# Kernel optimization log

Measured on AMD Instinct MI355X. Metric: run time of the kernel, lower is better.

The kernel has to match this reference:

```python
import jax, jax.numpy as jnp
import numpy as np

D_MODEL = 768
D_STATE = 16
K_CONV = 4
BATCH = 2
SEQ = 2048


def setup_inputs() -> dict:
    key = jax.random.key(0)
    ks = jax.random.split(key, 16)
    dm, ds, K = D_MODEL, D_STATE, K_CONV
    s = 0.02
    inp = {
        "x": jax.random.normal(ks[0], (BATCH, SEQ, dm), dtype=jnp.float32),
        # linear weights stored (in, out); y = x @ W + b (equivalent to torch Linear)
        "Wi": jax.random.normal(ks[1], (dm, 2 * dm), dtype=jnp.float32) * s,
        "bi": jnp.zeros((2 * dm,), jnp.float32),
        "Wconv": jax.random.normal(ks[2], (dm, K), dtype=jnp.float32) * s,
        "bconv": jnp.zeros((dm,), jnp.float32),
        "Wdt": jax.random.normal(ks[3], (dm, dm), dtype=jnp.float32) * s,
        "bdt": jnp.zeros((dm,), jnp.float32),
        "WB": jax.random.normal(ks[4], (dm, dm * ds), dtype=jnp.float32) * s,
        "bB": jnp.zeros((dm * ds,), jnp.float32),
        "WC": jax.random.normal(ks[5], (dm, dm * ds), dtype=jnp.float32) * s,
        "bC": jnp.zeros((dm * ds,), jnp.float32),
        "A_log": jnp.zeros((dm, ds), jnp.float32),  # matches nn.Parameter(torch.zeros)
        "D": jnp.ones((dm,), jnp.float32),          # matches nn.Parameter(torch.ones)
        "Wo": jax.random.normal(ks[6], (dm, dm), dtype=jnp.float32) * s,
        "bo": jnp.zeros((dm,), jnp.float32),
    }
    return inp


def _forward(x, Wi, bi, Wconv, bconv, Wdt, bdt, WB, bB, WC, bC, A_log, D, Wo, bo):
    B, L, dm = x.shape
    ds = A_log.shape[1]
    K = Wconv.shape[1]

    uv = x @ Wi + bi                        # (B, L, 2*dm)
    u, v = uv[..., :dm], uv[..., dm:]

    # causal depthwise conv1d: torch pads K-1 both sides, keeps first L outputs
    u_pad = jnp.pad(u, ((0, 0), (K - 1, 0), (0, 0)))
    u_conv = bconv + sum(u_pad[:, k:k + L, :] * Wconv[:, k] for k in range(K))

    dt = jax.nn.softplus(u_conv @ Wdt + bdt)            # (B, L, dm)
    Bt = (u_conv @ WB + bB).reshape(B, L, dm, ds)       # (B, L, dm, ds)
    Ct = (u_conv @ WC + bC).reshape(B, L, dm, ds)
    A = -jnp.exp(A_log)                                  # (dm, ds)

    def step(s, inputs):
        dt_t, u_t, B_tt, C_tt = inputs                   # (B,dm), (B,dm), (B,dm,ds), (B,dm,ds)
        dt_e = dt_t[..., None]
        s = s * jnp.exp(dt_e * A) + dt_e * B_tt * u_t[..., None]
        y = jnp.sum(C_tt * s, axis=-1) + D * u_t         # (B, dm)
        return s, y

    s0 = jnp.zeros((B, dm, ds), x.dtype)
    xs = (dt.transpose(1, 0, 2), u_conv.transpose(1, 0, 2),
          Bt.transpose(1, 0, 2, 3), Ct.transpose(1, 0, 2, 3))
    _, ys = jax.lax.scan(step, s0, xs)                   # ys: (L, B, dm)
    y = ys.transpose(1, 0, 2)

    y = y * jax.nn.sigmoid(v)
    return y @ Wo + bo


def reference(x, Wi, bi, Wconv, bconv, Wdt, bdt, WB, bB, WC, bC, A_log, D, Wo, bo):
    return _forward(x, Wi, bi, Wconv, bconv, Wdt, bdt, WB, bB, WC, bC, A_log, D, Wo, bo)
```

## Files before the change

### kernel.cpp

```cpp
#include <hip/hip_runtime.h>

#define DM 768
#define DS 16
#define SEQ 2048
#define BATCH 2
#define MROWS (BATCH*SEQ)
#define N_UV (2*DM)
#define N_BC (DM*DS)
#define NGRP (BATCH*DM/4)
#define SUBMAX 32

typedef _Float16 half8 __attribute__((ext_vector_type(8)));
typedef float floatx4 __attribute__((ext_vector_type(4)));

static __device__ __forceinline__ unsigned short f2h(float f) {
  _Float16 h = (_Float16)f;
  return __builtin_bit_cast(unsigned short, h);
}
static __device__ __forceinline__ float h2f(unsigned short u) {
  return (float)__builtin_bit_cast(_Float16, u);
}
static __device__ __forceinline__ float softplus_f(float x) {
  return (x > 20.f) ? x : log1pf(__expf(x));
}
static __device__ __forceinline__ void async_cp16(const unsigned short* g,
                                                  unsigned short* l) {
  __builtin_amdgcn_global_load_lds(
      (const __attribute__((address_space(1))) void*)g,
      (__attribute__((address_space(3))) void*)l, 16, 0, 0);
}
static __device__ __forceinline__ float row_reduce16(float v) {
  int x;
  x = __builtin_amdgcn_update_dpp(0, __builtin_bit_cast(int, v), 0x128, 0xf, 0xf, true);
  v += __builtin_bit_cast(float, x);
  x = __builtin_amdgcn_update_dpp(0, __builtin_bit_cast(int, v), 0x124, 0xf, 0xf, true);
  v += __builtin_bit_cast(float, x);
  x = __builtin_amdgcn_update_dpp(0, __builtin_bit_cast(int, v), 0x122, 0xf, 0xf, true);
  v += __builtin_bit_cast(float, x);
  x = __builtin_amdgcn_update_dpp(0, __builtin_bit_cast(int, v), 0x121, 0xf, 0xf, true);
  v += __builtin_bit_cast(float, x);
  return v;
}

__global__ void convert_f2h(const float* __restrict__ in,
                            unsigned short* __restrict__ out, int n) {
  int i = (blockIdx.x * blockDim.x + threadIdx.x) * 4;
  if (i >= n) return;
  float4 f = *(const float4*)(in + i);
  ushort4 h;
  h.x = f2h(f.x); h.y = f2h(f.y); h.z = f2h(f.z); h.w = f2h(f.w);
  *(ushort4*)(out + i) = h;
}

__global__ void transpose_f2h(const float* __restrict__ W,
                              unsigned short* __restrict__ WT, int K, int N) {
  __shared__ float tile[32][33];
  int n0 = blockIdx.x * 32, k0 = blockIdx.y * 32;
  int tx = threadIdx.x, ty = threadIdx.y;
#pragma unroll
  for (int i = 0; i < 32; i += 8)
    tile[ty + i][tx] = W[(size_t)(k0 + ty + i) * N + (n0 + tx)];
  __syncthreads();
#pragma unroll
  for (int i = 0; i < 32; i += 8)
    WT[(size_t)(n0 + ty + i) * K + (k0 + tx)] = f2h(tile[tx][ty + i]);
}

template<int ACT, int OUTH, int TRANS>
__global__ __launch_bounds__(256)
void gemm_f16(const unsigned short* __restrict__ A,
              const unsigned short* __restrict__ BT0,
              const unsigned short* __restrict__ BT1,
              const float* __restrict__ bias0,
              const float* __restrict__ bias1,
              void* __restrict__ Cout0,
              void* __restrict__ Cout1,
              int M, int N, int K, int TCa, int bstride, int row0, int ldT) {
  const unsigned short* BT = blockIdx.z ? BT1 : BT0;
  const float* bias = blockIdx.z ? bias1 : bias0;
  void* Cout = blockIdx.z ? Cout1 : Cout0;
  __shared__ __align__(16) unsigned short smem[2 * 128 * 32];
  unsigned short* As = smem;
  unsigned short* Bs = smem + 128 * 32;
  const int m0 = blockIdx.y * 128, n0 = blockIdx.x * 128;
  const int tid = threadIdx.x;
  const int lane = tid & 63, wave = tid >> 6;
  const int wm = (wave >> 1) * 64, wn = (wave & 1) * 64;
  const int l16 = lane & 15, quad = lane >> 4;
  const int sr = tid >> 2;
  const int sc = (((tid & 3) ^ ((tid >> 3) & 3))) * 8;
  const int pch = (quad ^ ((l16 >> 1) & 3)) * 8;

  floatx4 acc[4][4] = {};

  const int mA0 = m0 + sr, mA1 = m0 + sr + 64;
  const int gA0 = (mA0 / TCa) * bstride + row0 + (mA0 % TCa);
  const int gA1 = (mA1 / TCa) * bstride + row0 + (mA1 % TCa);
  const unsigned short* Arow0 = A + (size_t)gA0 * K + sc;
  const unsigned short* Arow1 = A + (size_t)gA1 * K + sc;
  const unsigned short* Brow0 = BT + (size_t)(n0 + sr) * K + sc;
  const unsigned short* Brow1 = BT + (size_t)(n0 + sr + 64) * K + sc;
  unsigned short* ldsA0 = As + (wave * 16) * 32;
  unsigned short* ldsA1 = As + (64 + wave * 16) * 32;
  unsigned short* ldsB0 = Bs + (wave * 16) * 32;
  unsigned short* ldsB1 = Bs + (64 + wave * 16) * 32;

  for (int k0 = 0; k0 < K; k0 += 32) {
    async_cp16(Arow0 + k0, ldsA0);
    async_cp16(Arow1 + k0, ldsA1);
    async_cp16(Brow0 + k0, ldsB0);
    async_cp16(Brow1 + k0, ldsB1);
    __syncthreads();
    half8 af[4], bf[4];
#pragma unroll
    for (int i = 0; i < 4; i++) {
      af[i] = __builtin_bit_cast(half8, *(const uint4*)&As[(wm + i * 16 + l16) * 32 + pch]);
      bf[i] = __builtin_bit_cast(half8, *(const uint4*)&Bs[(wn + i * 16 + l16) * 32 + pch]);
    }
#pragma unroll
    for (int mi = 0; mi < 4; mi++)
#pragma unroll
      for (int ni = 0; ni < 4; ni++)
        acc[mi][ni] = __builtin_amdgcn_mfma_f32_16x16x32_f16(af[mi], bf[ni], acc[mi][ni], 0, 0, 0);
    __syncthreads();
  }

  if (TRANS) {
#pragma unroll
    for (int ph = 0; ph < 2; ph++) {
      __syncthreads();
#pragma unroll
      for (int nn = 0; nn < 2; nn++) {
        int ni = ph * 2 + nn;
        int colb = wn + ni * 16 + l16;
        int cc = (wn >> 1) + nn * 16 + l16;
        float bv = bias[n0 + colb];
#pragma unroll
        for (int mi = 0; mi < 4; mi++) {
          int slot = (wm >> 2) + mi * 4 + quad;
          int pair = slot >> 1, bitb = slot & 1;
          int phys = ((pair ^ (cc & 15)) << 1) | bitb;
          union { _Float16 h[4]; unsigned long long u; } pk;
#pragma unroll
          for (int r = 0; r < 4; r++) {
            float v = acc[mi][ni][r] + bv;
            if (ACT == 1) v = softplus_f(v);
            pk.h[r] = (_Float16)v;
          }
          *(unsigned long long*)&smem[cc * 128 + phys * 4] = pk.u;
        }
      }
      __syncthreads();
#pragma unroll
      for (int pass = 0; pass < 4; pass++) {
        int cc = (tid >> 4) + pass * 16;
        int p16 = tid & 15;
        uint4 v = *(const uint4*)&smem[cc * 128 + (p16 ^ (cc & 15)) * 8];
        int colb = ((cc & 32) ? 64 : 0) + (ph * 2 + ((cc >> 4) & 1)) * 16 + (cc & 15);
        *(uint4*)&((unsigned short*)Cout)[(size_t)(n0 + colb) * ldT + m0 + p16 * 8] = v;
      }
    }
  } else {
#pragma unroll
    for (int ni = 0; ni < 4; ni++) {
      int col = n0 + wn + ni * 16 + l16;
      float bv = bias[col];
#pragma unroll
      for (int mi = 0; mi < 4; mi++) {
#pragma unroll
        for (int r = 0; r < 4; r++) {
          int row = m0 + wm + mi * 16 + quad * 4 + r;
          float v = acc[mi][ni][r] + bv;
          if (ACT == 1) v = softplus_f(v);
          if (OUTH) ((unsigned short*)Cout)[(size_t)row * N + col] = f2h(v);
          else      ((float*)Cout)[(size_t)row * N + col] = v;
        }
      }
    }
  }
}

__global__ void dwconv(const unsigned short* __restrict__ uv,
                       const float* __restrict__ Wconv,
                       const float* __restrict__ bconv,
                       unsigned short* __restrict__ uc) {
  int idx = blockIdx.x * 256 + threadIdx.x;
  int c = (idx % (DM / 2)) * 2;
  int row = idx / (DM / 2);
  int t = row & (SEQ - 1);
  float a0 = bconv[c], a1 = bconv[c + 1];
  const float* w0 = Wconv + c * 4;
  const float* w1 = Wconv + (c + 1) * 4;
#pragma unroll
  for (int k = 0; k < 4; k++) {
    int tt = t - 3 + k;
    if (tt >= 0) {
      ushort2 u2 = *(const ushort2*)&uv[(size_t)(row - 3 + k) * N_UV + c];
      a0 += h2f(u2.x) * w0[k];
      a1 += h2f(u2.y) * w1[k];
    }
  }
  ushort2 o; o.x = f2h(a0); o.y = f2h(a1);
  *(ushort2*)&uc[(size_t)row * DM + c] = o;
}

__global__ __launch_bounds__(64)
void scan_pass1(const unsigned short* __restrict__ dtT,
                const unsigned short* __restrict__ uc,
                const unsigned short* __restrict__ BtcT,
                const float* __restrict__ A_log,
                float* __restrict__ Ssub,
                float* __restrict__ Aexp,
                int ci, int TC, int SUBn) {
  const int TSUB = TC / SUBn;
  const int MC = BATCH * TC;
  int wid = blockIdx.x, sub = blockIdx.y;
  int b = wid / (DM / 4);
  int c0 = (wid % (DM / 4)) * 4;
  int lane = threadIdx.x;
  int c = c0 + (lane >> 4);
  float Acj = -__expf(A_log[c0 * DS + lane]);
  int col = c0 * DS + lane;
  size_t gbase = (size_t)b * SEQ + (size_t)ci * TC + (size_t)sub * TSUB;
  size_t lbase = (size_t)b * TC + (size_t)sub * TSUB;
  const unsigned short* pB = BtcT + (size_t)col * MC + lbase;
  const unsigned short* pD = dtT + (size_t)c * MROWS + gbase;

  float s = 0.f, dsum = 0.f;
  uint4 vB = *(const uint4*)pB;
  uint4 vD = *(const uint4*)pD;
  float n_u[8];
#pragma unroll
  for (int i = 0; i < 8; i++) n_u[i] = h2f(uc[(gbase + i) * DM + c]);

  for (int t0 = 0; t0 < TSUB; t0 += 8) {
    half8 hB = __builtin_bit_cast(half8, vB);
    half8 hD = __builtin_bit_cast(half8, vD);
    float c_u[8];
#pragma unroll
    for (int i = 0; i < 8; i++) c_u[i] = n_u[i];
    if (t0 + 8 < TSUB) {
      vB = *(const uint4*)(pB + t0 + 8);
      vD = *(const uint4*)(pD + t0 + 8);
#pragma unroll
      for (int i = 0; i < 8; i++) n_u[i] = h2f(uc[(gbase + t0 + 8 + i) * DM + c]);
    }
#pragma unroll
    for (int i = 0; i < 8; i++) {
      float dtc = (float)hD[i];
      dsum += dtc;
      float a = __expf(dtc * Acj);
      s = fmaf(s, a, dtc * (float)hB[i] * c_u[i]);
    }
  }
  int idx = (sub * BATCH + b) * N_BC + col;
  Ssub[idx] = s;
  Aexp[idx] = __expf(Acj * dsum);
}

__global__ __launch_bounds__(64)
void scan_combine(const float* __restrict__ Ssub, const float* __restrict__ Aexp,
                  float* __restrict__ Sinit, float* __restrict__ s_state,
                  int ci, int SUBn) {
  int wid = blockIdx.x;
  int b = wid / (DM / 4);
  int c0 = (wid % (DM / 4)) * 4;
  int col = c0 * DS + threadIdx.x;
  int sidx = b * N_BC + col;
  float s = (ci == 0) ? 0.f : s_state[sidx];
  for (int k = 0; k < SUBn; k++) {
    int idx = (k * BATCH + b) * N_BC + col;
    Sinit[idx] = s;
    s = fmaf(s, Aexp[idx], Ssub[idx]);
  }
  s_state[sidx] = s;
}

__global__ __launch_bounds__(64)
void scan_pass2(const unsigned short* __restrict__ dtT,
                const unsigned short* __restrict__ uc,
                const unsigned short* __restrict__ BtcT,
                const unsigned short* __restrict__ CtcT,
                const unsigned short* __restrict__ uv,
                const float* __restrict__ A_log,
                const float* __restrict__ Dv,
                const float* __restrict__ Sinit,
                unsigned short* __restrict__ yg,
                int ci, int TC, int SUBn) {
  const int TSUB = TC / SUBn;
  const int MC = BATCH * TC;
  int wid = blockIdx.x, sub = blockIdx.y;
  int b = wid / (DM / 4);
  int c0 = (wid % (DM / 4)) * 4;
  int lane = threadIdx.x;
  int j = lane & 15;
  int c = c0 + (lane >> 4);
  float Acj = -__expf(A_log[c0 * DS + lane]);
  float Dc = Dv[c];
  int col = c0 * DS + lane;
  float s = Sinit[(sub * BATCH + b) * N_BC + col];
  size_t gbase = (size_t)b * SEQ + (size_t)ci * TC + (size_t)sub * TSUB;
  size_t lbase = (size_t)b * TC + (size_t)sub * TSUB;
  const unsigned short* pB = BtcT + (size_t)col * MC + lbase;
  const unsigned short* pC = CtcT + (size_t)col * MC + lbase;
  const unsigned short* pD = dtT + (size_t)c * MROWS + gbase;

  uint4 vB = *(const uint4*)pB;
  uint4 vC = *(const uint4*)pC;
  uint4 vD = *(const uint4*)pD;
  float n_u[8], n_v[8];
#pragma unroll
  for (int i = 0; i < 8; i++) {
    n_u[i] = h2f(uc[(gbase + i) * DM + c]);
    n_v[i] = h2f(uv[(gbase + i) * N_UV + DM + c]);
  }

  for (int t0 = 0; t0 < TSUB; t0 += 8) {
    half8 hB = __builtin_bit_cast(half8, vB);
    half8 hC = __builtin_bit_cast(half8, vC);
    half8 hD = __builtin_bit_cast(half8, vD);
    float c_u[8], c_v[8];
#pragma unroll
    for (int i = 0; i < 8; i++) { c_u[i] = n_u[i]; c_v[i] = n_v[i]; }
    if (t0 + 8 < TSUB) {
      vB = *(const uint4*)(pB + t0 + 8);
      vC = *(const uint4*)(pC + t0 + 8);
      vD = *(const uint4*)(pD + t0 + 8);
#pragma unroll
      for (int i = 0; i < 8; i++) {
        n_u[i] = h2f(uc[(gbase + t0 + 8 + i) * DM + c]);
        n_v[i] = h2f(uv[(gbase + t0 + 8 + i) * N_UV + DM + c]);
      }
    }
#pragma unroll
    for (int i = 0; i < 8; i++) {
      float dtc = (float)hD[i];
      float a = __expf(dtc * Acj);
      s = fmaf(s, a, dtc * (float)hB[i] * c_u[i]);
      float yt = row_reduce16((float)hC[i] * s);
      if (j == 0) {
        float y = yt + Dc * c_u[i];
        float g = 1.f / (1.f + __expf(-c_v[i]));
        yg[(gbase + t0 + i) * DM + c] = f2h(y * g);
      }
    }
  }
}

extern "C" void kernel_launch(void* const* d_in, const int* in_sizes, int n_in,
                              void* d_out, int out_size, void* d_ws, size_t ws_size,
                              hipStream_t stream) {
  const float* x     = (const float*)d_in[0];
  const float* Wi    = (const float*)d_in[1];
  const float* bi    = (const float*)d_in[2];
  const float* Wconv = (const float*)d_in[3];
  const float* bconv = (const float*)d_in[4];
  const float* Wdt   = (const float*)d_in[5];
  const float* bdt   = (const float*)d_in[6];
  const float* WB    = (const float*)d_in[7];
  const float* bB    = (const float*)d_in[8];
  const float* WC    = (const float*)d_in[9];
  const float* bC    = (const float*)d_in[10];
  const float* A_log = (const float*)d_in[11];
  const float* Dv    = (const float*)d_in[12];
  const float* Wo    = (const float*)d_in[13];
  const float* bo    = (const float*)d_in[14];
  float* out = (float*)d_out;
  (void)in_sizes; (void)n_in; (void)out_size;

  auto pad = [](size_t b) { return (b + 255) & ~(size_t)255; };

  const size_t sz_xb   = pad((size_t)MROWS * DM * 2);
  const size_t sz_WiT  = pad((size_t)N_UV * DM * 2);
  const size_t sz_WdtT = pad((size_t)DM * DM * 2);
  const size_t sz_WBT  = pad((size_t)N_BC * DM * 2);
  const size_t sz_WCT  = pad((size_t)N_BC * DM * 2);
  const size_t sz_WoT  = pad((size_t)DM * DM * 2);
  const size_t sz_uvb  = pad((size_t)MROWS * N_UV * 2);
  const size_t sz_ucb  = pad((size_t)MROWS * DM * 2);
  const size_t sz_dtb  = pad((size_t)MROWS * DM * 2);
  const size_t sz_st   = pad((size_t)BATCH * N_BC * 4);
  const size_t sz_sub  = pad((size_t)SUBMAX * BATCH * N_BC * 4);
  const size_t fixed = sz_xb + sz_WiT + sz_WdtT + sz_WBT + sz_WCT + sz_WoT +
                       sz_uvb + sz_ucb + sz_dtb + sz_st + 3 * sz_sub;

  int NC = 16;
  for (int nc : {1, 2, 4, 8, 16}) {
    size_t need = fixed + 2 * pad((size_t)BATCH * (SEQ / nc) * N_BC * 2);
    if (need <= ws_size) { NC = nc; break; }
  }
  const int TC = SEQ / NC;
  const int MC = BATCH * TC;
  const int SUBn = (TC / 8 < SUBMAX) ? (TC / 8) : SUBMAX;

  char* ws = (char*)d_ws;
  size_t off = 0;
  auto alloc = [&](size_t bytes) { char* p = ws + off; off += bytes; return p; };
  unsigned short* xb   = (unsigned short*)alloc(sz_xb);
  unsigned short* WiT  = (unsigned short*)alloc(sz_WiT);
  unsigned short* WdtT = (unsigned short*)alloc(sz_WdtT);
  unsigned short* WBT  = (unsigned short*)alloc(sz_WBT);
  unsigned short* WCT  = (unsigned short*)alloc(sz_WCT);
  unsigned short* WoT  = (unsigned short*)alloc(sz_WoT);
  unsigned short* uvb  = (unsigned short*)alloc(sz_uvb);
  unsigned short* ucb  = (unsigned short*)alloc(sz_ucb);
  unsigned short* dtb  = (unsigned short*)alloc(sz_dtb);
  float*          sst  = (float*)alloc(sz_st);
  float*          Ssub = (float*)alloc(sz_sub);
  float*          Aexp = (float*)alloc(sz_sub);
  float*          Sini = (float*)alloc(sz_sub);
  unsigned short* Btc  = (unsigned short*)alloc(pad((size_t)MC * N_BC * 2));
  unsigned short* Ctc  = (unsigned short*)alloc(pad((size_t)MC * N_BC * 2));
  unsigned short* ygb  = xb;

  convert_f2h<<<dim3(MROWS * DM / 1024), dim3(256), 0, stream>>>(x, xb, MROWS * DM);
  transpose_f2h<<<dim3(N_UV / 32, DM / 32), dim3(32, 8), 0, stream>>>(Wi, WiT, DM, N_UV);
  transpose_f2h<<<dim3(DM / 32, DM / 32), dim3(32, 8), 0, stream>>>(Wdt, WdtT, DM, DM);
  transpose_f2h<<<dim3(N_BC / 32, DM / 32), dim3(32, 8), 0, stream>>>(WB, WBT, DM, N_BC);
  transpose_f2h<<<dim3(N_BC / 32, DM / 32), dim3(32, 8), 0, stream>>>(WC, WCT, DM, N_BC);
  transpose_f2h<<<dim3(DM / 32, DM / 32), dim3(32, 8), 0, stream>>>(Wo, WoT, DM, DM);

  gemm_f16<0, 1, 0><<<dim3(N_UV / 128, MROWS / 128, 1), 256, 0, stream>>>(
      xb, WiT, WiT, bi, bi, uvb, uvb, MROWS, N_UV, DM, MROWS, 0, 0, 0);
  dwconv<<<dim3(MROWS * DM / 512), 256, 0, stream>>>(uvb, Wconv, bconv, ucb);
  gemm_f16<1, 1, 1><<<dim3(DM / 128, MROWS / 128, 1), 256, 0, stream>>>(
      ucb, WdtT, WdtT, bdt, bdt, dtb, dtb, MROWS, DM, DM, MROWS, 0, 0, MROWS);

  for (int ci = 0; ci < NC; ci++) {
    gemm_f16<0, 1, 1><<<dim3(N_BC / 128, MC / 128, 2), 256, 0, stream>>>(
        ucb, WBT, WCT, bB, bC, Btc, Ctc, MC, N_BC, DM, TC, SEQ, ci * TC, MC);
    scan_pass1<<<dim3(NGRP, SUBn), 64, 0, stream>>>(dtb, ucb, Btc, A_log, Ssub, Aexp, ci, TC, SUBn);
    scan_combine<<<dim3(NGRP), 64, 0, stream>>>(Ssub, Aexp, Sini, sst, ci, SUBn);
    scan_pass2<<<dim3(NGRP, SUBn), 64, 0, stream>>>(dtb, ucb, Btc, Ctc, uvb,
                                                    A_log, Dv, Sini, ygb, ci, TC, SUBn);
  }

  gemm_f16<0, 0, 0><<<dim3(DM / 128, MROWS / 128, 1), 256, 0, stream>>>(
      ygb, WoT, WoT, bo, bo, out, out, MROWS, DM, DM, MROWS, 0, 0, 0);
}
```

Baseline: 688.3 us.

## Transpose u and v to time-major layout, pad strides, and merge weight transposes

Adds transpose kernels so the scan passes read u_conv and the v gate as contiguous 16-byte vectors along time instead of strided scalar loads, matching the existing layout of dt, B and C. It also pads the leading dimensions of the transposed buffers by 8 elements to avoid power-of-two strides, and merges the five weight transpose launches into one kernel with packed 32-bit stores. The cost is two extra transpose passes over activations and more workspace, which may lower the chunk count NC chosen for the B/C buffers.

```diff
diff --git a/kernel.cpp b/kernel.cpp
--- a/kernel.cpp
+++ b/kernel.cpp
@@ -5,6 +5,7 @@
 #define SEQ 2048
 #define BATCH 2
 #define MROWS (BATCH*SEQ)
+#define MR8 (MROWS+8)
 #define N_UV (2*DM)
 #define N_BC (DM*DS)
 #define NGRP (BATCH*DM/4)
@@ -52,18 +53,58 @@
   *(ushort4*)(out + i) = h;
 }
 
-__global__ void transpose_f2h(const float* __restrict__ W,
-                              unsigned short* __restrict__ WT, int K, int N) {
+__global__ void transpose_w5(const float* __restrict__ W0, const float* __restrict__ W1,
+                             const float* __restrict__ W2, const float* __restrict__ W3,
+                             const float* __restrict__ W4,
+                             unsigned short* __restrict__ T0, unsigned short* __restrict__ T1,
+                             unsigned short* __restrict__ T2, unsigned short* __restrict__ T3,
+                             unsigned short* __restrict__ T4,
+                             int N0, int N1, int N2, int N3, int N4) {
+  const float* W; unsigned short* WT; int N;
+  switch (blockIdx.z) {
+    case 0: W = W0; WT = T0; N = N0; break;
+    case 1: W = W1; WT = T1; N = N1; break;
+    case 2: W = W2; WT = T2; N = N2; break;
+    case 3: W = W3; WT = T3; N = N3; break;
+    default: W = W4; WT = T4; N = N4; break;
+  }
+  int n0 = blockIdx.x * 32;
+  if (n0 >= N) return;
+  int k0 = blockIdx.y * 32;
   __shared__ float tile[32][33];
-  int n0 = blockIdx.x * 32, k0 = blockIdx.y * 32;
   int tx = threadIdx.x, ty = threadIdx.y;
 #pragma unroll
   for (int i = 0; i < 32; i += 8)
     tile[ty + i][tx] = W[(size_t)(k0 + ty + i) * N + (n0 + tx)];
   __syncthreads();
-#pragma unroll
-  for (int i = 0; i < 32; i += 8)
-    WT[(size_t)(n0 + ty + i) * K + (k0 + tx)] = f2h(tile[tx][ty + i]);
+  int kp = tx & 15, half = tx >> 4;
+#pragma unroll
+  for (int i = 0; i < 2; i++) {
+    int nl = ty + half * 8 + i * 16;
+    unsigned int pk = (unsigned int)f2h(tile[2 * kp][nl]) |
+                      ((unsigned int)f2h(tile[2 * kp + 1][nl]) << 16);
+    *(unsigned int*)&WT[(size_t)(n0 + nl) * DM + k0 + 2 * kp] = pk;
+  }
+}
+
+__global__ void transpose_h(const unsigned short* __restrict__ src, int src_ld,
+                            unsigned short* __restrict__ dst, int dst_ld) {
+  __shared__ __align__(16) unsigned short tile[64][72];
+  int t0 = blockIdx.x * 64, c0 = blockIdx.y * 64;
+  int tid = threadIdx.x;
+  int lr = tid >> 3, lc = (tid & 7) * 8;
+#pragma unroll
+  for (int rr = 0; rr < 64; rr += 32)
+    *(uint4*)&tile[rr + lr][lc] = *(const uint4*)&src[(size_t)(t0 + rr + lr) * src_ld + c0 + lc];
+  __syncthreads();
+  int sc = tid >> 3, st = (tid & 7) * 8;
+#pragma unroll
+  for (int cc = 0; cc < 64; cc += 32) {
+    union { unsigned short h[8]; uint4 v; } pk;
+#pragma unroll
+    for (int i = 0; i < 8; i++) pk.h[i] = tile[st + i][cc + sc];
+    *(uint4*)&dst[(size_t)(c0 + cc + sc) * dst_ld + t0 + st] = pk.v;
+  }
 }
 
 template<int ACT, int OUTH, int TRANS>
@@ -206,14 +247,12 @@
 
 __global__ __launch_bounds__(64)
 void scan_pass1(const unsigned short* __restrict__ dtT,
-                const unsigned short* __restrict__ uc,
+                const unsigned short* __restrict__ ucT,
                 const unsigned short* __restrict__ BtcT,
                 const float* __restrict__ A_log,
-                float* __restrict__ Ssub,
-                float* __restrict__ Aexp,
-                int ci, int TC, int SUBn) {
+                float* __restrict__ Ssub, float* __restrict__ Aexp,
+                int ci, int TC, int SUBn, int MC8) {
   const int TSUB = TC / SUBn;
-  const int MC = BATCH * TC;
   int wid = blockIdx.x, sub = blockIdx.y;
   int b = wid / (DM / 4);
   int c0 = (wid % (DM / 4)) * 4;
@@ -223,34 +262,29 @@
   int col = c0 * DS + lane;
   size_t gbase = (size_t)b * SEQ + (size_t)ci * TC + (size_t)sub * TSUB;
   size_t lbase = (size_t)b * TC + (size_t)sub * TSUB;
-  const unsigned short* pB = BtcT + (size_t)col * MC + lbase;
-  const unsigned short* pD = dtT + (size_t)c * MROWS + gbase;
+  const unsigned short* pB = BtcT + (size_t)col * MC8 + lbase;
+  const unsigned short* pD = dtT + (size_t)c * MR8 + gbase;
+  const unsigned short* pU = ucT + (size_t)c * MR8 + gbase;
 
   float s = 0.f, dsum = 0.f;
   uint4 vB = *(const uint4*)pB;
   uint4 vD = *(const uint4*)pD;
-  float n_u[8];
-#pragma unroll
-  for (int i = 0; i < 8; i++) n_u[i] = h2f(uc[(gbase + i) * DM + c]);
-
+  uint4 vU = *(const uint4*)pU;
   for (int t0 = 0; t0 < TSUB; t0 += 8) {
     half8 hB = __builtin_bit_cast(half8, vB);
     half8 hD = __builtin_bit_cast(half8, vD);
-    float c_u[8];
-#pragma unroll
-    for (int i = 0; i < 8; i++) c_u[i] = n_u[i];
+    half8 hU = __builtin_bit_cast(half8, vU);
     if (t0 + 8 < TSUB) {
       vB = *(const uint4*)(pB + t0 + 8);
       vD = *(const uint4*)(pD + t0 + 8);
-#pragma unroll
-      for (int i = 0; i < 8; i++) n_u[i] = h2f(uc[(gbase + t0 + 8 + i) * DM + c]);
+      vU = *(const uint4*)(pU + t0 + 8);
     }
 #pragma unroll
     for (int i = 0; i < 8; i++) {
       float dtc = (float)hD[i];
       dsum += dtc;
       float a = __expf(dtc * Acj);
-      s = fmaf(s, a, dtc * (float)hB[i] * c_u[i]);
+      s = fmaf(s, a, dtc * (float)hB[i] * (float)hU[i]);
     }
   }
   int idx = (sub * BATCH + b) * N_BC + col;
@@ -278,17 +312,16 @@
 
 __global__ __launch_bounds__(64)
 void scan_pass2(const unsigned short* __restrict__ dtT,
-                const unsigned short* __restrict__ uc,
+                const unsigned short* __restrict__ ucT,
                 const unsigned short* __restrict__ BtcT,
                 const unsigned short* __restrict__ CtcT,
-                const unsigned short* __restrict__ uv,
+                const unsigned short* __restrict__ vT,
                 const float* __restrict__ A_log,
                 const float* __restrict__ Dv,
                 const float* __restrict__ Sinit,
                 unsigned short* __restrict__ yg,
-                int ci, int TC, int SUBn) {
+                int ci, int TC, int SUBn, int MC8) {
   const int TSUB = TC / SUBn;
-  const int MC = BATCH * TC;
   int wid = blockIdx.x, sub = blockIdx.y;
   int b = wid / (DM / 4);
   int c0 = (wid % (DM / 4)) * 4;
@@ -301,46 +334,40 @@
   float s = Sinit[(sub * BATCH + b) * N_BC + col];
   size_t gbase = (size_t)b * SEQ + (size_t)ci * TC + (size_t)sub * TSUB;
   size_t lbase = (size_t)b * TC + (size_t)sub * TSUB;
-  const unsigned short* pB = BtcT + (size_t)col * MC + lbase;
-  const unsigned short* pC = CtcT + (size_t)col * MC + lbase;
-  const unsigned short* pD = dtT + (size_t)c * MROWS + gbase;
+  const unsigned short* pB = BtcT + (size_t)col * MC8 + lbase;
+  const unsigned short* pC = CtcT + (size_t)col * MC8 + lbase;
+  const unsigned short* pD = dtT + (size_t)c * MR8 + gbase;
+  const unsigned short* pU = ucT + (size_t)c * MR8 + gbase;
+  const unsigned short* pV = vT + (size_t)c * MR8 + gbase;
 
   uint4 vB = *(const uint4*)pB;
   uint4 vC = *(const uint4*)pC;
   uint4 vD = *(const uint4*)pD;
-  float n_u[8], n_v[8];
-#pragma unroll
-  for (int i = 0; i < 8; i++) {
-    n_u[i] = h2f(uc[(gbase + i) * DM + c]);
-    n_v[i] = h2f(uv[(gbase + i) * N_UV + DM + c]);
-  }
-
+  uint4 vU = *(const uint4*)pU;
+  uint4 vV = *(const uint4*)pV;
   for (int t0 = 0; t0 < TSUB; t0 += 8) {
     half8 hB = __builtin_bit_cast(half8, vB);
     half8 hC = __builtin_bit_cast(half8, vC);
     half8 hD = __builtin_bit_cast(half8, vD);
-    float c_u[8], c_v[8];
-#pragma unroll
-    for (int i = 0; i < 8; i++) { c_u[i] = n_u[i]; c_v[i] = n_v[i]; }
+    half8 hU = __builtin_bit_cast(half8, vU);
+    half8 hV = __builtin_bit_cast(half8, vV);
     if (t0 + 8 < TSUB) {
       vB = *(const uint4*)(pB + t0 + 8);
       vC = *(const uint4*)(pC + t0 + 8);
       vD = *(const uint4*)(pD + t0 + 8);
-#pragma unroll
-      for (int i = 0; i < 8; i++) {
-        n_u[i] = h2f(uc[(gbase + t0 + 8 + i) * DM + c]);
-        n_v[i] = h2f(uv[(gbase + t0 + 8 + i) * N_UV + DM + c]);
-      }
+      vU = *(const uint4*)(pU + t0 + 8);
+      vV = *(const uint4*)(pV + t0 + 8);
     }
 #pragma unroll
     for (int i = 0; i < 8; i++) {
       float dtc = (float)hD[i];
+      float uu = (float)hU[i];
       float a = __expf(dtc * Acj);
-      s = fmaf(s, a, dtc * (float)hB[i] * c_u[i]);
+      s = fmaf(s, a, dtc * (float)hB[i] * uu);
       float yt = row_reduce16((float)hC[i] * s);
       if (j == 0) {
-        float y = yt + Dc * c_u[i];
-        float g = 1.f / (1.f + __expf(-c_v[i]));
+        float y = yt + Dc * uu;
+        float g = 1.f / (1.f + __expf(-(float)hV[i]));
         yg[(gbase + t0 + i) * DM + c] = f2h(y * g);
       }
     }
@@ -378,19 +405,20 @@
   const size_t sz_WoT  = pad((size_t)DM * DM * 2);
   const size_t sz_uvb  = pad((size_t)MROWS * N_UV * 2);
   const size_t sz_ucb  = pad((size_t)MROWS * DM * 2);
-  const size_t sz_dtb  = pad((size_t)MROWS * DM * 2);
+  const size_t sz_tr   = pad((size_t)DM * MR8 * 2);
   const size_t sz_st   = pad((size_t)BATCH * N_BC * 4);
   const size_t sz_sub  = pad((size_t)SUBMAX * BATCH * N_BC * 4);
   const size_t fixed = sz_xb + sz_WiT + sz_WdtT + sz_WBT + sz_WCT + sz_WoT +
-                       sz_uvb + sz_ucb + sz_dtb + sz_st + 3 * sz_sub;
+                       sz_uvb + sz_ucb + 3 * sz_tr + sz_st + 3 * sz_sub;
 
   int NC = 16;
   for (int nc : {1, 2, 4, 8, 16}) {
-    size_t need = fixed + 2 * pad((size_t)BATCH * (SEQ / nc) * N_BC * 2);
+    size_t need = fixed + 2 * pad((size_t)N_BC * (BATCH * (SEQ / nc) + 8) * 2);
     if (need <= ws_size) { NC = nc; break; }
   }
   const int TC = SEQ / NC;
   const int MC = BATCH * TC;
+  const int MC8 = MC + 8;
   const int SUBn = (TC / 8 < SUBMAX) ? (TC / 8) : SUBMAX;
 
   char* ws = (char*)d_ws;
@@ -404,35 +432,37 @@
   unsigned short* WoT  = (unsigned short*)alloc(sz_WoT);
   unsigned short* uvb  = (unsigned short*)alloc(sz_uvb);
   unsigned short* ucb  = (unsigned short*)alloc(sz_ucb);
-  unsigned short* dtb  = (unsigned short*)alloc(sz_dtb);
+  unsigned short* dtT  = (unsigned short*)alloc(sz_tr);
+  unsigned short* ucT  = (unsigned short*)alloc(sz_tr);
+  unsigned short* vT   = (unsigned short*)alloc(sz_tr);
   float*          sst  = (float*)alloc(sz_st);
   float*          Ssub = (float*)alloc(sz_sub);
   float*          Aexp = (float*)alloc(sz_sub);
   float*          Sini = (float*)alloc(sz_sub);
-  unsigned short* Btc  = (unsigned short*)alloc(pad((size_t)MC * N_BC * 2));
-  unsigned short* Ctc  = (unsigned short*)alloc(pad((size_t)MC * N_BC * 2));
+  unsigned short* Btc  = (unsigned short*)alloc(pad((size_t)N_BC * MC8 * 2));
+  unsigned short* Ctc  = (unsigned short*)alloc(pad((size_t)N_BC * MC8 * 2));
   unsigned short* ygb  = xb;
 
   convert_f2h<<<dim3(MROWS * DM / 1024), dim3(256), 0, stream>>>(x, xb, MROWS * DM);
-  transpose_f2h<<<dim3(N_UV / 32, DM / 32), dim3(32, 8), 0, stream>>>(Wi, WiT, DM, N_UV);
-  transpose_f2h<<<dim3(DM / 32, DM / 32), dim3(32, 8), 0, stream>>>(Wdt, WdtT, DM, DM);
-  transpose_f2h<<<dim3(N_BC / 32, DM / 32), dim3(32, 8), 0, stream>>>(WB, WBT, DM, N_BC);
-  transpose_f2h<<<dim3(N_BC / 32, DM / 32), dim3(32, 8), 0, stream>>>(WC, WCT, DM, N_BC);
-  transpose_f2h<<<dim3(DM / 32, DM / 32), dim3(32, 8), 0, stream>>>(Wo, WoT, DM, DM);
+  transpose_w5<<<dim3(N_BC / 32, DM / 32, 5), dim3(32, 8), 0, stream>>>(
+      Wi, Wdt, WB, WC, Wo, WiT, WdtT, WBT, WCT, WoT, N_UV, DM, N_BC, N_BC, DM);
 
   gemm_f16<0, 1, 0><<<dim3(N_UV / 128, MROWS / 128, 1), 256, 0, stream>>>(
       xb, WiT, WiT, bi, bi, uvb, uvb, MROWS, N_UV, DM, MROWS, 0, 0, 0);
   dwconv<<<dim3(MROWS * DM / 512), 256, 0, stream>>>(uvb, Wconv, bconv, ucb);
+  transpose_h<<<dim3(MROWS / 64, DM / 64), 256, 0, stream>>>(ucb, DM, ucT, MR8);
+  transpose_h<<<dim3(MROWS / 64, DM / 64), 256, 0, stream>>>(uvb + DM, N_UV, vT, MR8);
   gemm_f16<1, 1, 1><<<dim3(DM / 128, MROWS / 128, 1), 256, 0, stream>>>(
-      ucb, WdtT, WdtT, bdt, bdt, dtb, dtb, MROWS, DM, DM, MROWS, 0, 0, MROWS);
+      ucb, WdtT, WdtT, bdt, bdt, dtT, dtT, MROWS, DM, DM, MROWS, 0, 0, MR8);
 
   for (int ci = 0; ci < NC; ci++) {
     gemm_f16<0, 1, 1><<<dim3(N_BC / 128, MC / 128, 2), 256, 0, stream>>>(
-        ucb, WBT, WCT, bB, bC, Btc, Ctc, MC, N_BC, DM, TC, SEQ, ci * TC, MC);
-    scan_pass1<<<dim3(NGRP, SUBn), 64, 0, stream>>>(dtb, ucb, Btc, A_log, Ssub, Aexp, ci, TC, SUBn);
+        ucb, WBT, WCT, bB, bC, Btc, Ctc, MC, N_BC, DM, TC, SEQ, ci * TC, MC8);
+    scan_pass1<<<dim3(NGRP, SUBn), 64, 0, stream>>>(dtT, ucT, Btc, A_log,
+                                                    Ssub, Aexp, ci, TC, SUBn, MC8);
     scan_combine<<<dim3(NGRP), 64, 0, stream>>>(Ssub, Aexp, Sini, sst, ci, SUBn);
-    scan_pass2<<<dim3(NGRP, SUBn), 64, 0, stream>>>(dtb, ucb, Btc, Ctc, uvb,
-                                                    A_log, Dv, Sini, ygb, ci, TC, SUBn);
+    scan_pass2<<<dim3(NGRP, SUBn), 64, 0, stream>>>(dtT, ucT, Btc, Ctc, vT,
+                                                    A_log, Dv, Sini, ygb, ci, TC, SUBn, MC8);
   }
 
   gemm_f16<0, 0, 0><<<dim3(DM / 128, MROWS / 128, 1), 256, 0, stream>>>(
```

Measured after the change: 667.0 us. 3.1% less time.
